# Optimization experiments

Measured on AMD Instinct MI355X. Metric: run time of the kernel, lower is better.

The kernel has to match this reference:

```python
import jax, jax.numpy as jnp
import numpy as np

N = 100000          # nodes
E = 1600000         # edges (avg degree 16)
D_IN = 128
D_OUT = 128
K = 3               # Chebyshev order
LAMBDA_MAX = 2.0    # PyG default for sym normalization


def setup_inputs() -> dict:
    key = jax.random.key(0)
    k1, k2, k3, k4 = jax.random.split(key, 4)
    x = jax.random.normal(k1, (N, D_IN), dtype=jnp.float32)
    edge_index = jax.random.randint(k2, (2, E), 0, N, dtype=jnp.int32)
    # Glorot-ish init for the K per-order linear weights
    weight = jax.random.normal(k3, (K, D_IN, D_OUT), dtype=jnp.float32) * (1.0 / np.sqrt(D_IN))
    bias = jax.random.normal(k4, (D_OUT,), dtype=jnp.float32) * 0.01
    return {"x": x, "edge_index": edge_index, "weight": weight, "bias": bias}


def reference(x, edge_index, weight, bias):
    src, dst = edge_index[0], edge_index[1]
    n = x.shape[0]

    # remove self loops (zero their weight), symmetric normalization
    ew = jnp.where(src != dst, 1.0, 0.0).astype(x.dtype)
    deg = jax.ops.segment_sum(ew, src, num_segments=n)
    dis = jnp.where(deg > 0, jax.lax.rsqrt(jnp.maximum(deg, 1.0)), 0.0)
    norm = dis[src] * ew * dis[dst]          # D^-1/2 A D^-1/2 entries

    # scaled Laplacian T-hat = (2/lmax) L - I, L = I - A_norm
    off_w = -(2.0 / LAMBDA_MAX) * norm       # off-diagonal entries
    diag_w = 2.0 / LAMBDA_MAX - 1.0          # = 0 for lambda_max=2

    def spmm(h):  # T-hat @ h : gather-multiply-scatter over edges
        agg = jax.ops.segment_sum(off_w[:, None] * h[src], dst, num_segments=n)
        return agg + diag_w * h

    # Chebyshev recurrence: Tx_k = 2 T-hat Tx_{k-1} - Tx_{k-2}
    Tx0 = x
    out = Tx0 @ weight[0]
    Tx1 = spmm(Tx0)
    out = out + Tx1 @ weight[1]
    for k in range(2, weight.shape[0]):
        Tx2 = 2.0 * spmm(Tx1) - Tx0
        out = out + Tx2 @ weight[k]
        Tx0, Tx1 = Tx1, Tx2
    return out + bias
```

## Files before the change

kernel.cpp:

```cpp
#include <hip/hip_runtime.h>
#include <hip/hip_bf16.h>

typedef __hip_bfloat16 bf16;
typedef __attribute__((ext_vector_type(8))) short short8;
typedef __attribute__((ext_vector_type(4))) float float4v;
typedef __attribute__((ext_vector_type(2))) float float2v;

#define N_NODES 100000
#define M_PAD   100096
#define N_EDGES 1600000
#define D 128
#define K_CAT 384
#define BUCKET_CAP 56
#define NBIN 392
#define BIN_CAP 4608
#define CHUNK 2048
#define NCHUNKA 782

__device__ __forceinline__ float b2f(bf16 v) { return __bfloat162float(v); }
__device__ __forceinline__ bf16 f2b(float v) { return __float2bfloat16(v); }
__device__ __forceinline__ float ub(unsigned int u, int k) {
    return (float)((u >> (k * 8)) & 0xffu);
}
__device__ __forceinline__ float2v cvt2lo(unsigned int u) {
    float a, b;
    asm("v_cvt_f32_ubyte0 %0, %2\n\t"
        "v_cvt_f32_ubyte1 %1, %2"
        : "=&v"(a), "=&v"(b) : "v"(u));
    float2v o; o.x = a; o.y = b; return o;
}
__device__ __forceinline__ float2v cvt2hi(unsigned int u) {
    float a, b;
    asm("v_cvt_f32_ubyte2 %0, %2\n\t"
        "v_cvt_f32_ubyte3 %1, %2"
        : "=&v"(a), "=&v"(b) : "v"(u));
    float2v o; o.x = a; o.y = b; return o;
}

__global__ void prep_w_kernel(const float* __restrict__ w, const float* __restrict__ bias,
                              bf16* __restrict__ wT, float* __restrict__ biasf) {
    int i = blockIdx.x * blockDim.x + threadIdx.x;
    if (i < D * K_CAT) {
        int o = i / K_CAT, k = i % K_CAT;
        float v;
        if (k < 128) {
            v = w[k * D + o] - w[2 * 16384 + k * D + o];
        } else if (k < 256) {
            v = w[16384 + (k - 128) * D + o];
        } else {
            v = 2.0f * w[2 * 16384 + (k - 256) * D + o];
        }
        wT[i] = f2b(v);
    }
    if (i < D) biasf[i] = bias[i];
}

__global__ __launch_bounds__(256) void quantx_kernel(const float* __restrict__ x,
                                                     const float* __restrict__ dis,
                                                     unsigned char* __restrict__ xq,
                                                     float* __restrict__ dsx0) {
    int wv = threadIdx.x >> 6, lane = threadIdx.x & 63;
    int n = blockIdx.x * 4 + wv;
    float2 v = *(const float2*)(x + (size_t)n * D + lane * 2);
    float m = fmaxf(fabsf(v.x), fabsf(v.y));
#pragma unroll
    for (int k = 1; k < 64; k <<= 1) m = fmaxf(m, __shfl_xor(m, k));
    float inv = (m > 0.0f) ? 127.0f / m : 0.0f;
    int q0 = (int)rintf(v.x * inv) + 128;
    int q1 = (int)rintf(v.y * inv) + 128;
    *(unsigned short*)(xq + (size_t)n * D + lane * 2) =
        (unsigned short)((q0 & 0xff) | ((q1 & 0xff) << 8));
    if (lane == 0) dsx0[n] = dis[n] * (m * (1.0f / 127.0f));
}

__global__ __launch_bounds__(256) void phaseA_kernel(const int* __restrict__ src,
                                                     const int* __restrict__ dst,
                                                     int* __restrict__ gCursD,
                                                     int* __restrict__ gCursS,
                                                     unsigned int* __restrict__ gBinD,
                                                     unsigned char* __restrict__ gBinS) {
    __shared__ int hist[NBIN], curs[NBIN];
    int tid = threadIdx.x;
    int b = blockIdx.x;
    int sideS = (b >= NCHUNKA);
    int e0 = (sideS ? b - NCHUNKA : b) * CHUNK;
    for (int t = tid; t < NBIN; t += 256) hist[t] = 0;
    __syncthreads();
    for (int i = tid; i < CHUNK; i += 256) {
        int e = e0 + i;
        if (e >= N_EDGES) break;
        int s = src[e], d = dst[e];
        if (s == d) continue;
        atomicAdd(&hist[(sideS ? s : d) >> 8], 1);
    }
    __syncthreads();
    int* gC = sideS ? gCursS : gCursD;
    for (int t = tid; t < NBIN; t += 256)
        curs[t] = (hist[t] > 0) ? atomicAdd(&gC[t], hist[t]) : 0;
    __syncthreads();
    for (int i = tid; i < CHUNK; i += 256) {
        int e = e0 + i;
        if (e >= N_EDGES) break;
        int s = src[e], d = dst[e];
        if (s == d) continue;
        if (!sideS) {
            int bd = d >> 8;
            int sd = atomicAdd(&curs[bd], 1);
            if (sd < BIN_CAP) gBinD[(size_t)bd * BIN_CAP + sd] = ((unsigned int)s << 8) | (unsigned int)(d & 255);
        } else {
            int bs = s >> 8;
            int ss = atomicAdd(&curs[bs], 1);
            if (ss < BIN_CAP) gBinS[(size_t)bs * BIN_CAP + ss] = (unsigned char)(s & 255);
        }
    }
}

__global__ __launch_bounds__(256) void phaseB_kernel(const int* __restrict__ gCursD,
                                                     const int* __restrict__ gCursS,
                                                     const unsigned int* __restrict__ gBinD,
                                                     const unsigned char* __restrict__ gBinS,
                                                     int* __restrict__ cnt,
                                                     float* __restrict__ dis,
                                                     int* __restrict__ bucket) {
    __shared__ int curs[256];
    int tid = threadIdx.x;
    int b = blockIdx.x;
    curs[tid] = 0;
    __syncthreads();
    if (b < NBIN) {
        int count = min(gCursD[b], BIN_CAP);
        const unsigned int* rec = gBinD + (size_t)b * BIN_CAP;
        int n0 = b << 8;
        for (int j = tid; j < count; j += 256) {
            unsigned int r = rec[j];
            int dloc = r & 255;
            int s = (int)(r >> 8);
            int slot = atomicAdd(&curs[dloc], 1);
            if (slot < BUCKET_CAP) bucket[(size_t)(n0 + dloc) * BUCKET_CAP + slot] = s;
        }
        __syncthreads();
        int n = n0 + tid;
        if (n < N_NODES) cnt[n] = curs[tid];
    } else {
        int bb = b - NBIN;
        int count = min(gCursS[bb], BIN_CAP);
        const unsigned char* rec = gBinS + (size_t)bb * BIN_CAP;
        for (int j = tid; j < count; j += 256) {
            atomicAdd(&curs[rec[j]], 1);
        }
        __syncthreads();
        int n = (bb << 8) + tid;
        if (n < N_NODES) {
            int c = curs[tid];
            dis[n] = (c > 0) ? rsqrtf((float)c) : 0.0f;
        }
    }
}

template<int OUTQ>
__global__ __launch_bounds__(256) void spmm_q_kernel(const unsigned char* __restrict__ hq,
                                                     const float* __restrict__ dsx,
                                                     const float* __restrict__ dis,
                                                     const int* __restrict__ cnt,
                                                     const int* __restrict__ bucket,
                                                     unsigned char* __restrict__ outq,
                                                     float* __restrict__ oscale,
                                                     float* __restrict__ odsx,
                                                     bf16* __restrict__ outb) {
    int wv = threadIdx.x >> 6;
    int lane = threadIdx.x & 63;
    int n = blockIdx.x * 4 + wv;
    int c = min(cnt[n], BUCKET_CAP);
    float dn = dis[n];
    int q = lane >> 4;
    int r = lane & 15;
    int s_l = 0;
    float w_l = 0.0f;
    if (lane < c) {
        s_l = bucket[(size_t)n * BUCKET_CAP + lane];
        w_l = -dsx[s_l] * dn;
    }
    const unsigned char* hr = hq + (r << 3);

    float2v acc2[4];
#pragma unroll
    for (int k = 0; k < 4; k++) acc2[k] = (float2v)0.0f;
    float cw = 0.0f;

    int sA = __shfl(s_l, q), sB = __shfl(s_l, 4 + q);
    float wA = __shfl(w_l, q), wB = __shfl(w_l, 4 + q);
    uint2 uA = *(const uint2*)(hr + (size_t)sA * D);
    uint2 uB = *(const uint2*)(hr + (size_t)sB * D);

    for (int j0 = 0; j0 < c; j0 += 8) {
        int nj = j0 + 8;
        int sA2 = __shfl(s_l, nj + q);
        int sB2 = __shfl(s_l, nj + 4 + q);
        float wA2 = __shfl(w_l, nj + q);
        float wB2 = __shfl(w_l, nj + 4 + q);
        uint2 uA2 = *(const uint2*)(hr + (size_t)sA2 * D);
        uint2 uB2 = *(const uint2*)(hr + (size_t)sB2 * D);
        cw += wA + wB;
        float2v wAv; wAv.x = wA; wAv.y = wA;
        float2v wBv; wBv.x = wB; wBv.y = wB;
        acc2[0] += wAv * cvt2lo(uA.x);
        acc2[1] += wAv * cvt2hi(uA.x);
        acc2[2] += wAv * cvt2lo(uA.y);
        acc2[3] += wAv * cvt2hi(uA.y);
        acc2[0] += wBv * cvt2lo(uB.x);
        acc2[1] += wBv * cvt2hi(uB.x);
        acc2[2] += wBv * cvt2lo(uB.y);
        acc2[3] += wBv * cvt2hi(uB.y);
        sA = sA2; sB = sB2; wA = wA2; wB = wB2; uA = uA2; uB = uB2;
    }

    float acc[8];
#pragma unroll
    for (int k = 0; k < 4; k++) { acc[2 * k] = acc2[k].x; acc[2 * k + 1] = acc2[k].y; }
#pragma unroll
    for (int k = 0; k < 8; k++) {
        acc[k] += __shfl_xor(acc[k], 16);
        acc[k] += __shfl_xor(acc[k], 32);
    }
    cw += __shfl_xor(cw, 16);
    cw += __shfl_xor(cw, 32);
#pragma unroll
    for (int k = 0; k < 8; k++) acc[k] -= 128.0f * cw;

    if (OUTQ) {
        float m = 0.0f;
#pragma unroll
        for (int k = 0; k < 8; k++) m = fmaxf(m, fabsf(acc[k]));
#pragma unroll
        for (int k = 1; k < 16; k <<= 1) m = fmaxf(m, __shfl_xor(m, k));
        float inv = (m > 0.0f) ? 127.0f / m : 0.0f;
        if (q == 0) {
            unsigned int b0 = 0, b1 = 0;
#pragma unroll
            for (int k = 0; k < 4; k++)
                b0 |= ((unsigned int)((int)rintf(acc[k] * inv) + 128) & 0xffu) << (8 * k);
#pragma unroll
            for (int k = 0; k < 4; k++)
                b1 |= ((unsigned int)((int)rintf(acc[4 + k] * inv) + 128) & 0xffu) << (8 * k);
            uint2 pk; pk.x = b0; pk.y = b1;
            *(uint2*)(outq + (size_t)n * D + (r << 3)) = pk;
            if (lane == 0) {
                float sc = m * (1.0f / 127.0f);
                oscale[n] = sc;
                odsx[n] = dn * sc;
            }
        }
    } else {
        if (q == 0) {
            unsigned int p0 = (unsigned int)__bfloat16_as_ushort(f2b(acc[0])) |
                              ((unsigned int)__bfloat16_as_ushort(f2b(acc[1])) << 16);
            unsigned int p1 = (unsigned int)__bfloat16_as_ushort(f2b(acc[2])) |
                              ((unsigned int)__bfloat16_as_ushort(f2b(acc[3])) << 16);
            unsigned int p2 = (unsigned int)__bfloat16_as_ushort(f2b(acc[4])) |
                              ((unsigned int)__bfloat16_as_ushort(f2b(acc[5])) << 16);
            unsigned int p3 = (unsigned int)__bfloat16_as_ushort(f2b(acc[6])) |
                              ((unsigned int)__bfloat16_as_ushort(f2b(acc[7])) << 16);
            uint4 pk; pk.x = p0; pk.y = p1; pk.z = p2; pk.w = p3;
            *(uint4*)(outb + (size_t)n * D + (r << 3)) = pk;
        }
    }
}

#define AS_STRIDE 40
__global__ __launch_bounds__(256) void gemm_kernel(const float* __restrict__ x,
                                                   const unsigned char* __restrict__ tx1q,
                                                   const float* __restrict__ tx1scale,
                                                   const bf16* __restrict__ agg2,
                                                   const bf16* __restrict__ wT,
                                                   const float* __restrict__ biasf,
                                                   float* __restrict__ out) {
    __shared__ bf16 As[128 * AS_STRIDE];
    __shared__ bf16 Bs[128 * AS_STRIDE];

    int tid = threadIdx.x;
    int nb = blockIdx.x * 128;
    int w = tid >> 6;
    int lane = tid & 63;
    int lq = lane >> 4;
    int lr = lane & 15;

    float4v acc[2][8];
#pragma unroll
    for (int i = 0; i < 2; i++)
#pragma unroll
        for (int j = 0; j < 8; j++) acc[i][j] = (float4v)0.0f;

    for (int kc = 0; kc < 12; kc++) {
        int kbase = kc * 32;
        if (kc < 4) {
#pragma unroll
            for (int t = 0; t < 4; t++) {
                int c = tid + t * 256;
                int row = c >> 3;
                int off = (c & 7) * 4;
                int gr = nb + row;
                if (gr > N_NODES - 1) gr = N_NODES - 1;
                float4 v = *(const float4*)(x + (size_t)gr * D + kbase + off);
                unsigned int p0 = (unsigned int)__bfloat16_as_ushort(f2b(v.x)) |
                                  ((unsigned int)__bfloat16_as_ushort(f2b(v.y)) << 16);
                unsigned int p1 = (unsigned int)__bfloat16_as_ushort(f2b(v.z)) |
                                  ((unsigned int)__bfloat16_as_ushort(f2b(v.w)) << 16);
                uint2 pk; pk.x = p0; pk.y = p1;
                *(uint2*)(As + row * AS_STRIDE + off) = pk;
            }
        } else if (kc < 8) {
            int soff = (kc & 3) * 32;
#pragma unroll
            for (int t = 0; t < 2; t++) {
                int c = tid + t * 256;
                int row = c >> 2;
                int off = (c & 3) * 8;
                int gr = nb + row;
                uint2 u = *(const uint2*)(tx1q + (size_t)gr * D + soff + off);
                float sc = tx1scale[gr];
                float f0 = sc * (ub(u.x, 0) - 128.0f);
                float f1 = sc * (ub(u.x, 1) - 128.0f);
                float f2 = sc * (ub(u.x, 2) - 128.0f);
                float f3 = sc * (ub(u.x, 3) - 128.0f);
                float f4 = sc * (ub(u.y, 0) - 128.0f);
                float f5 = sc * (ub(u.y, 1) - 128.0f);
                float f6 = sc * (ub(u.y, 2) - 128.0f);
                float f7 = sc * (ub(u.y, 3) - 128.0f);
                uint4 pk;
                pk.x = (unsigned int)__bfloat16_as_ushort(f2b(f0)) |
                       ((unsigned int)__bfloat16_as_ushort(f2b(f1)) << 16);
                pk.y = (unsigned int)__bfloat16_as_ushort(f2b(f2)) |
                       ((unsigned int)__bfloat16_as_ushort(f2b(f3)) << 16);
                pk.z = (unsigned int)__bfloat16_as_ushort(f2b(f4)) |
                       ((unsigned int)__bfloat16_as_ushort(f2b(f5)) << 16);
                pk.w = (unsigned int)__bfloat16_as_ushort(f2b(f6)) |
                       ((unsigned int)__bfloat16_as_ushort(f2b(f7)) << 16);
                *(uint4*)(As + row * AS_STRIDE + off) = pk;
            }
        } else {
            int soff = (kc & 3) * 32;
#pragma unroll
            for (int t = 0; t < 2; t++) {
                int c = tid + t * 256;
                int row = c >> 2;
                int off = (c & 3) * 8;
                uint4 v = *(const uint4*)(agg2 + (size_t)(nb + row) * D + soff + off);
                *(uint4*)(As + row * AS_STRIDE + off) = v;
            }
        }
#pragma unroll
        for (int t = 0; t < 2; t++) {
            int c = tid + t * 256;
            int row = c >> 2;
            int off = (c & 3) * 8;
            uint4 v = *(const uint4*)(wT + (size_t)row * K_CAT + kbase + off);
            *(uint4*)(Bs + row * AS_STRIDE + off) = v;
        }
        __syncthreads();

        short8 af[2], bfr[8];
#pragma unroll
        for (int i = 0; i < 2; i++)
            af[i] = *(const short8*)(As + (w * 32 + i * 16 + lr) * AS_STRIDE + lq * 8);
#pragma unroll
        for (int j = 0; j < 8; j++)
            bfr[j] = *(const short8*)(Bs + (j * 16 + lr) * AS_STRIDE + lq * 8);
#pragma unroll
        for (int i = 0; i < 2; i++)
#pragma unroll
            for (int j = 0; j < 8; j++)
                acc[i][j] = __builtin_amdgcn_mfma_f32_16x16x32_bf16(af[i], bfr[j], acc[i][j], 0, 0, 0);
        __syncthreads();
    }

#pragma unroll
    for (int i = 0; i < 2; i++) {
        int rowb = nb + w * 32 + i * 16 + lq * 4;
#pragma unroll
        for (int j = 0; j < 8; j++) {
            int col = j * 16 + lr;
            float bv = biasf[col];
#pragma unroll
            for (int r = 0; r < 4; r++) {
                int row = rowb + r;
                if (row < N_NODES) out[(size_t)row * D + col] = acc[i][j][r] + bv;
            }
        }
    }
}

extern "C" void kernel_launch(void* const* d_in, const int* in_sizes, int n_in,
                              void* d_out, int out_size, void* d_ws, size_t ws_size,
                              hipStream_t stream) {
    const float* x    = (const float*)d_in[0];
    const int*   ei   = (const int*)d_in[1];
    const float* w    = (const float*)d_in[2];
    const float* bias = (const float*)d_in[3];
    float* out = (float*)d_out;

    char* p = (char*)d_ws;
    int*   cnt      = (int*)p;     p += (size_t)N_NODES * 4;
    float* dis      = (float*)p;   p += (size_t)N_NODES * 4;
    int*   gCurs    = (int*)p;     p += (size_t)2 * NBIN * 4;
    float* dsx0     = (float*)p;   p += (size_t)M_PAD * 4;
    float* tx1scale = (float*)p;   p += (size_t)M_PAD * 4;
    float* dsx1     = (float*)p;   p += (size_t)M_PAD * 4;
    int*   bucket   = (int*)p;     p += (size_t)N_NODES * BUCKET_CAP * 4;
    char*  buf1     = p;           p += (size_t)M_PAD * D * 2;
    bf16*  buf2     = (bf16*)p;    p += (size_t)M_PAD * D * 2;
    bf16*  wT       = (bf16*)p;    p += (size_t)D * K_CAT * 2;
    float* biasf    = (float*)p;   p += (size_t)D * 4;

    int*   gCursD = gCurs;
    int*   gCursS = gCurs + NBIN;
    unsigned int*  gBinD = (unsigned int*)buf1;
    unsigned char* gBinS = (unsigned char*)(gBinD + (size_t)NBIN * BIN_CAP);
    unsigned char* xq   = (unsigned char*)buf1;
    unsigned char* tx1q = xq + (size_t)M_PAD * D;
    bf16* agg2 = buf2;

    hipMemsetAsync(gCurs, 0, (size_t)2 * NBIN * 4, stream);

    prep_w_kernel<<<(D * K_CAT + 255) / 256, 256, 0, stream>>>(w, bias, wT, biasf);
    phaseA_kernel<<<2 * NCHUNKA, 256, 0, stream>>>(ei, ei + N_EDGES,
                                                   gCursD, gCursS, gBinD, gBinS);
    phaseB_kernel<<<2 * NBIN, 256, 0, stream>>>(gCursD, gCursS, gBinD, gBinS, cnt, dis, bucket);
    quantx_kernel<<<N_NODES / 4, 256, 0, stream>>>(x, dis, xq, dsx0);
    spmm_q_kernel<1><<<N_NODES / 4, 256, 0, stream>>>(xq, dsx0, dis, cnt, bucket,
                                                      tx1q, tx1scale, dsx1, (bf16*)nullptr);
    spmm_q_kernel<0><<<N_NODES / 4, 256, 0, stream>>>(tx1q, dsx1, dis, cnt, bucket,
                                                      (unsigned char*)nullptr, (float*)nullptr,
                                                      (float*)nullptr, agg2);
    gemm_kernel<<<M_PAD / 128, 256, 0, stream>>>(x, tx1q, tx1scale, agg2, wT, biasf, out);
}
```

Baseline: 333.7 us.

## Fuse prep into phaseA, quantize x inside phaseB, feed GEMM with int8 x

Folds the weight-prep kernel into the edge binning kernel as extra blocks. A single pass per chunk now builds both the dst and src histograms, replacing separate blocks for each side. The x quantization moves into the src-side phaseB blocks, and the GEMM reads the int8 x plus a per-row scale instead of fp32 x, which cuts launches and GEMM input traffic. In exchange, the x term in the output is now quantized to int8, which lowers accuracy, and the fused quantization is serialized over 64 nodes per wave.

```diff
diff --git a/kernel.cpp b/kernel.cpp
--- a/kernel.cpp
+++ b/kernel.cpp
@@ -14,10 +14,10 @@
 #define BUCKET_CAP 56
 #define NBIN 392
 #define BIN_CAP 4608
-#define CHUNK 2048
-#define NCHUNKA 782
-
-__device__ __forceinline__ float b2f(bf16 v) { return __bfloat162float(v); }
+#define CHUNK 4096
+#define NCHUNK 391
+#define PREPB 192
+
 __device__ __forceinline__ bf16 f2b(float v) { return __float2bfloat16(v); }
 __device__ __forceinline__ float ub(unsigned int u, int k) {
     return (float)((u >> (k * 8)) & 0xffu);
@@ -37,10 +37,20 @@
     float2v o; o.x = a; o.y = b; return o;
 }
 
-__global__ void prep_w_kernel(const float* __restrict__ w, const float* __restrict__ bias,
-                              bf16* __restrict__ wT, float* __restrict__ biasf) {
-    int i = blockIdx.x * blockDim.x + threadIdx.x;
-    if (i < D * K_CAT) {
+__global__ __launch_bounds__(256) void phaseA_prep_kernel(const int* __restrict__ src,
+                                                          const int* __restrict__ dst,
+                                                          const float* __restrict__ w,
+                                                          const float* __restrict__ bias,
+                                                          int* __restrict__ gCursD,
+                                                          int* __restrict__ gCursS,
+                                                          unsigned int* __restrict__ gBinD,
+                                                          unsigned char* __restrict__ gBinS,
+                                                          bf16* __restrict__ wT,
+                                                          float* __restrict__ biasf) {
+    __shared__ int histD[NBIN], histS[NBIN], cursD[NBIN], cursS[NBIN];
+    int tid = threadIdx.x;
+    if (blockIdx.x >= NCHUNK) {
+        int i = (blockIdx.x - NCHUNK) * 256 + tid;
         int o = i / K_CAT, k = i % K_CAT;
         float v;
         if (k < 128) {
@@ -51,77 +61,50 @@
             v = 2.0f * w[2 * 16384 + (k - 256) * D + o];
         }
         wT[i] = f2b(v);
-    }
-    if (i < D) biasf[i] = bias[i];
-}
-
-__global__ __launch_bounds__(256) void quantx_kernel(const float* __restrict__ x,
-                                                     const float* __restrict__ dis,
-                                                     unsigned char* __restrict__ xq,
-                                                     float* __restrict__ dsx0) {
-    int wv = threadIdx.x >> 6, lane = threadIdx.x & 63;
-    int n = blockIdx.x * 4 + wv;
-    float2 v = *(const float2*)(x + (size_t)n * D + lane * 2);
-    float m = fmaxf(fabsf(v.x), fabsf(v.y));
-#pragma unroll
-    for (int k = 1; k < 64; k <<= 1) m = fmaxf(m, __shfl_xor(m, k));
-    float inv = (m > 0.0f) ? 127.0f / m : 0.0f;
-    int q0 = (int)rintf(v.x * inv) + 128;
-    int q1 = (int)rintf(v.y * inv) + 128;
-    *(unsigned short*)(xq + (size_t)n * D + lane * 2) =
-        (unsigned short)((q0 & 0xff) | ((q1 & 0xff) << 8));
-    if (lane == 0) dsx0[n] = dis[n] * (m * (1.0f / 127.0f));
-}
-
-__global__ __launch_bounds__(256) void phaseA_kernel(const int* __restrict__ src,
-                                                     const int* __restrict__ dst,
-                                                     int* __restrict__ gCursD,
-                                                     int* __restrict__ gCursS,
-                                                     unsigned int* __restrict__ gBinD,
-                                                     unsigned char* __restrict__ gBinS) {
-    __shared__ int hist[NBIN], curs[NBIN];
-    int tid = threadIdx.x;
-    int b = blockIdx.x;
-    int sideS = (b >= NCHUNKA);
-    int e0 = (sideS ? b - NCHUNKA : b) * CHUNK;
-    for (int t = tid; t < NBIN; t += 256) hist[t] = 0;
+        if (i < D) biasf[i] = bias[i];
+        return;
+    }
+    for (int t = tid; t < NBIN; t += 256) { histD[t] = 0; histS[t] = 0; }
+    __syncthreads();
+    int e0 = blockIdx.x * CHUNK;
+    for (int i = tid; i < CHUNK; i += 256) {
+        int e = e0 + i;
+        if (e >= N_EDGES) break;
+        int s = src[e], d = dst[e];
+        if (s == d) continue;
+        atomicAdd(&histD[d >> 8], 1);
+        atomicAdd(&histS[s >> 8], 1);
+    }
+    __syncthreads();
+    for (int t = tid; t < NBIN; t += 256) {
+        cursD[t] = (histD[t] > 0) ? atomicAdd(&gCursD[t], histD[t]) : 0;
+        cursS[t] = (histS[t] > 0) ? atomicAdd(&gCursS[t], histS[t]) : 0;
+    }
     __syncthreads();
     for (int i = tid; i < CHUNK; i += 256) {
         int e = e0 + i;
         if (e >= N_EDGES) break;
         int s = src[e], d = dst[e];
         if (s == d) continue;
-        atomicAdd(&hist[(sideS ? s : d) >> 8], 1);
-    }
-    __syncthreads();
-    int* gC = sideS ? gCursS : gCursD;
-    for (int t = tid; t < NBIN; t += 256)
-        curs[t] = (hist[t] > 0) ? atomicAdd(&gC[t], hist[t]) : 0;
-    __syncthreads();
-    for (int i = tid; i < CHUNK; i += 256) {
-        int e = e0 + i;
-        if (e >= N_EDGES) break;
-        int s = src[e], d = dst[e];
-        if (s == d) continue;
-        if (!sideS) {
-            int bd = d >> 8;
-            int sd = atomicAdd(&curs[bd], 1);
-            if (sd < BIN_CAP) gBinD[(size_t)bd * BIN_CAP + sd] = ((unsigned int)s << 8) | (unsigned int)(d & 255);
-        } else {
-            int bs = s >> 8;
-            int ss = atomicAdd(&curs[bs], 1);
-            if (ss < BIN_CAP) gBinS[(size_t)bs * BIN_CAP + ss] = (unsigned char)(s & 255);
-        }
-    }
-}
-
-__global__ __launch_bounds__(256) void phaseB_kernel(const int* __restrict__ gCursD,
-                                                     const int* __restrict__ gCursS,
-                                                     const unsigned int* __restrict__ gBinD,
-                                                     const unsigned char* __restrict__ gBinS,
-                                                     int* __restrict__ cnt,
-                                                     float* __restrict__ dis,
-                                                     int* __restrict__ bucket) {
+        int bd = d >> 8, bs = s >> 8;
+        int sd = atomicAdd(&cursD[bd], 1);
+        if (sd < BIN_CAP) gBinD[(size_t)bd * BIN_CAP + sd] = ((unsigned int)s << 8) | (unsigned int)(d & 255);
+        int ss = atomicAdd(&cursS[bs], 1);
+        if (ss < BIN_CAP) gBinS[(size_t)bs * BIN_CAP + ss] = (unsigned char)(s & 255);
+    }
+}
+
+__global__ __launch_bounds__(256) void phaseBq_kernel(const int* __restrict__ gCursD,
+                                                      const int* __restrict__ gCursS,
+                                                      const unsigned int* __restrict__ gBinD,
+                                                      const unsigned char* __restrict__ gBinS,
+                                                      const float* __restrict__ x,
+                                                      int* __restrict__ cnt,
+                                                      float* __restrict__ dis,
+                                                      int* __restrict__ bucket,
+                                                      unsigned char* __restrict__ xq,
+                                                      float* __restrict__ xscale,
+                                                      float* __restrict__ dsx0) {
     __shared__ int curs[256];
     int tid = threadIdx.x;
     int b = blockIdx.x;
@@ -149,10 +132,32 @@
             atomicAdd(&curs[rec[j]], 1);
         }
         __syncthreads();
-        int n = (bb << 8) + tid;
+        int n0 = bb << 8;
+        int n = n0 + tid;
         if (n < N_NODES) {
             int c = curs[tid];
             dis[n] = (c > 0) ? rsqrtf((float)c) : 0.0f;
+        }
+        int wv = tid >> 6, lane = tid & 63;
+        for (int i = 0; i < 64; i++) {
+            int nn = n0 + wv * 64 + i;
+            if (nn >= N_NODES) break;
+            float2 v = *(const float2*)(x + (size_t)nn * D + lane * 2);
+            float m = fmaxf(fabsf(v.x), fabsf(v.y));
+#pragma unroll
+            for (int k = 1; k < 64; k <<= 1) m = fmaxf(m, __shfl_xor(m, k));
+            float inv = (m > 0.0f) ? 127.0f / m : 0.0f;
+            int q0 = (int)rintf(v.x * inv) + 128;
+            int q1 = (int)rintf(v.y * inv) + 128;
+            *(unsigned short*)(xq + (size_t)nn * D + lane * 2) =
+                (unsigned short)((q0 & 0xff) | ((q1 & 0xff) << 8));
+            if (lane == 0) {
+                float sc = m * (1.0f / 127.0f);
+                int cc = curs[wv * 64 + i];
+                float dnn = (cc > 0) ? rsqrtf((float)cc) : 0.0f;
+                xscale[nn] = sc;
+                dsx0[nn] = dnn * sc;
+            }
         }
     }
 }
@@ -267,7 +272,43 @@
 }
 
 #define AS_STRIDE 40
-__global__ __launch_bounds__(256) void gemm_kernel(const float* __restrict__ x,
+__device__ __forceinline__ void stage_q8(bf16* __restrict__ As,
+                                         const unsigned char* __restrict__ srcq,
+                                         const float* __restrict__ scl,
+                                         int nb, int kb) {
+    int tid = threadIdx.x;
+#pragma unroll
+    for (int t = 0; t < 2; t++) {
+        int c = tid + t * 256;
+        int row = c >> 2;
+        int off = (c & 3) * 8;
+        int gr = nb + row;
+        if (gr > N_NODES - 1) gr = N_NODES - 1;
+        uint2 u = *(const uint2*)(srcq + (size_t)gr * D + kb + off);
+        float sc = scl[gr];
+        float f0 = sc * (ub(u.x, 0) - 128.0f);
+        float f1 = sc * (ub(u.x, 1) - 128.0f);
+        float f2 = sc * (ub(u.x, 2) - 128.0f);
+        float f3 = sc * (ub(u.x, 3) - 128.0f);
+        float f4 = sc * (ub(u.y, 0) - 128.0f);
+        float f5 = sc * (ub(u.y, 1) - 128.0f);
+        float f6 = sc * (ub(u.y, 2) - 128.0f);
+        float f7 = sc * (ub(u.y, 3) - 128.0f);
+        uint4 pk;
+        pk.x = (unsigned int)__bfloat16_as_ushort(f2b(f0)) |
+               ((unsigned int)__bfloat16_as_ushort(f2b(f1)) << 16);
+        pk.y = (unsigned int)__bfloat16_as_ushort(f2b(f2)) |
+               ((unsigned int)__bfloat16_as_ushort(f2b(f3)) << 16);
+        pk.z = (unsigned int)__bfloat16_as_ushort(f2b(f4)) |
+               ((unsigned int)__bfloat16_as_ushort(f2b(f5)) << 16);
+        pk.w = (unsigned int)__bfloat16_as_ushort(f2b(f6)) |
+               ((unsigned int)__bfloat16_as_ushort(f2b(f7)) << 16);
+        *(uint4*)(As + row * AS_STRIDE + off) = pk;
+    }
+}
+
+__global__ __launch_bounds__(256) void gemm_kernel(const unsigned char* __restrict__ xq,
+                                                   const float* __restrict__ xscale,
                                                    const unsigned char* __restrict__ tx1q,
                                                    const float* __restrict__ tx1scale,
                                                    const bf16* __restrict__ agg2,
@@ -293,50 +334,9 @@
     for (int kc = 0; kc < 12; kc++) {
         int kbase = kc * 32;
         if (kc < 4) {
-#pragma unroll
-            for (int t = 0; t < 4; t++) {
-                int c = tid + t * 256;
-                int row = c >> 3;
-                int off = (c & 7) * 4;
-                int gr = nb + row;
-                if (gr > N_NODES - 1) gr = N_NODES - 1;
-                float4 v = *(const float4*)(x + (size_t)gr * D + kbase + off);
-                unsigned int p0 = (unsigned int)__bfloat16_as_ushort(f2b(v.x)) |
-                                  ((unsigned int)__bfloat16_as_ushort(f2b(v.y)) << 16);
-                unsigned int p1 = (unsigned int)__bfloat16_as_ushort(f2b(v.z)) |
-                                  ((unsigned int)__bfloat16_as_ushort(f2b(v.w)) << 16);
-                uint2 pk; pk.x = p0; pk.y = p1;
-                *(uint2*)(As + row * AS_STRIDE + off) = pk;
-            }
+            stage_q8(As, xq, xscale, nb, kc * 32);
         } else if (kc < 8) {
-            int soff = (kc & 3) * 32;
-#pragma unroll
-            for (int t = 0; t < 2; t++) {
-                int c = tid + t * 256;
-                int row = c >> 2;
-                int off = (c & 3) * 8;
-                int gr = nb + row;
-                uint2 u = *(const uint2*)(tx1q + (size_t)gr * D + soff + off);
-                float sc = tx1scale[gr];
-                float f0 = sc * (ub(u.x, 0) - 128.0f);
-                float f1 = sc * (ub(u.x, 1) - 128.0f);
-                float f2 = sc * (ub(u.x, 2) - 128.0f);
-                float f3 = sc * (ub(u.x, 3) - 128.0f);
-                float f4 = sc * (ub(u.y, 0) - 128.0f);
-                float f5 = sc * (ub(u.y, 1) - 128.0f);
-                float f6 = sc * (ub(u.y, 2) - 128.0f);
-                float f7 = sc * (ub(u.y, 3) - 128.0f);
-                uint4 pk;
-                pk.x = (unsigned int)__bfloat16_as_ushort(f2b(f0)) |
-                       ((unsigned int)__bfloat16_as_ushort(f2b(f1)) << 16);
-                pk.y = (unsigned int)__bfloat16_as_ushort(f2b(f2)) |
-                       ((unsigned int)__bfloat16_as_ushort(f2b(f3)) << 16);
-                pk.z = (unsigned int)__bfloat16_as_ushort(f2b(f4)) |
-                       ((unsigned int)__bfloat16_as_ushort(f2b(f5)) << 16);
-                pk.w = (unsigned int)__bfloat16_as_ushort(f2b(f6)) |
-                       ((unsigned int)__bfloat16_as_ushort(f2b(f7)) << 16);
-                *(uint4*)(As + row * AS_STRIDE + off) = pk;
-            }
+            stage_q8(As, tx1q, tx1scale, nb, (kc - 4) * 32);
         } else {
             int soff = (kc & 3) * 32;
 #pragma unroll
@@ -403,11 +403,13 @@
     float* dis      = (float*)p;   p += (size_t)N_NODES * 4;
     int*   gCurs    = (int*)p;     p += (size_t)2 * NBIN * 4;
     float* dsx0     = (float*)p;   p += (size_t)M_PAD * 4;
+    float* xscale   = (float*)p;   p += (size_t)M_PAD * 4;
     float* tx1scale = (float*)p;   p += (size_t)M_PAD * 4;
     float* dsx1     = (float*)p;   p += (size_t)M_PAD * 4;
     int*   bucket   = (int*)p;     p += (size_t)N_NODES * BUCKET_CAP * 4;
-    char*  buf1     = p;           p += (size_t)M_PAD * D * 2;
-    bf16*  buf2     = (bf16*)p;    p += (size_t)M_PAD * D * 2;
+    char*  buf1     = p;           p += (size_t)M_PAD * D;
+    unsigned char* xq = (unsigned char*)p; p += (size_t)M_PAD * D;
+    bf16*  agg2     = (bf16*)p;    p += (size_t)M_PAD * D * 2;
     bf16*  wT       = (bf16*)p;    p += (size_t)D * K_CAT * 2;
     float* biasf    = (float*)p;   p += (size_t)D * 4;
 
@@ -415,21 +417,20 @@
     int*   gCursS = gCurs + NBIN;
     unsigned int*  gBinD = (unsigned int*)buf1;
     unsigned char* gBinS = (unsigned char*)(gBinD + (size_t)NBIN * BIN_CAP);
-    unsigned char* xq   = (unsigned char*)buf1;
-    unsigned char* tx1q = xq + (size_t)M_PAD * D;
-    bf16* agg2 = buf2;
+    unsigned char* tx1q  = (unsigned char*)buf1;
 
     hipMemsetAsync(gCurs, 0, (size_t)2 * NBIN * 4, stream);
 
-    prep_w_kernel<<<(D * K_CAT + 255) / 256, 256, 0, stream>>>(w, bias, wT, biasf);
-    phaseA_kernel<<<2 * NCHUNKA, 256, 0, stream>>>(ei, ei + N_EDGES,
-                                                   gCursD, gCursS, gBinD, gBinS);
-    phaseB_kernel<<<2 * NBIN, 256, 0, stream>>>(gCursD, gCursS, gBinD, gBinS, cnt, dis, bucket);
-    quantx_kernel<<<N_NODES / 4, 256, 0, stream>>>(x, dis, xq, dsx0);
+    phaseA_prep_kernel<<<NCHUNK + PREPB, 256, 0, stream>>>(ei, ei + N_EDGES, w, bias,
+                                                           gCursD, gCursS, gBinD, gBinS,
+                                                           wT, biasf);
+    phaseBq_kernel<<<2 * NBIN, 256, 0, stream>>>(gCursD, gCursS, gBinD, gBinS, x,
+                                                 cnt, dis, bucket, xq, xscale, dsx0);
     spmm_q_kernel<1><<<N_NODES / 4, 256, 0, stream>>>(xq, dsx0, dis, cnt, bucket,
                                                       tx1q, tx1scale, dsx1, (bf16*)nullptr);
     spmm_q_kernel<0><<<N_NODES / 4, 256, 0, stream>>>(tx1q, dsx1, dis, cnt, bucket,
                                                       (unsigned char*)nullptr, (float*)nullptr,
                                                       (float*)nullptr, agg2);
-    gemm_kernel<<<M_PAD / 128, 256, 0, stream>>>(x, tx1q, tx1scale, agg2, wT, biasf, out);
-}
+    gemm_kernel<<<M_PAD / 128, 256, 0, stream>>>(xq, xscale, tx1q, tx1scale,
+                                                 agg2, wT, biasf, out);
+}
```

After: 353.4 us. +5.9%, slower.
